# Kernel optimization log

Hardware: AMD Instinct MI355X
Metric: run time of the kernel (lower is better)

The kernel has to match this reference:

```python
import jax, jax.numpy as jnp
import numpy as np

N, M, D, O = 16384, 4096, 256, 256

def setup_inputs() -> dict:
    key = jax.random.key(0)
    k1, k2, k3, k4, k5, k6, k7 = jax.random.split(key, 7)
    H_fine = jax.random.normal(k1, (N, D), dtype=jnp.float32)
    H_coarse = jax.random.normal(k2, (M, D), dtype=jnp.float32)
    inter_channel_adj = jax.random.randint(k3, (N, M), 0, 2).astype(jnp.float32)
    # attention = nn.Linear(2D, 1): weight vector [2D], bias scalar
    wa = jax.random.normal(k4, (2 * D,), dtype=jnp.float32) * (1.0 / np.sqrt(2 * D))
    ba = jax.random.normal(k5, (1,), dtype=jnp.float32) * 0.01
    # transform = nn.Linear(D, O), xavier_uniform weight
    lim = np.sqrt(6.0 / (D + O)).astype(np.float32)
    Wt = jax.random.uniform(k6, (O, D), minval=-lim, maxval=lim, dtype=jnp.float32)
    bt = jax.random.normal(k7, (O,), dtype=jnp.float32) * 0.01
    return {"H_fine": H_fine, "H_coarse": H_coarse,
            "inter_channel_adj": inter_channel_adj,
            "wa": wa, "ba": ba, "Wt": Wt, "bt": bt}

def reference(H_fine, H_coarse, inter_channel_adj, wa, ba, Wt, bt):
    d = H_fine.shape[-1]
    # additive attention: score_ij = [hf_i ; hc_j] . wa + b
    # = hf_i . wa[:d] + hc_j . wa[d:] + b  (avoids [N,M,2D] concat)
    sf = H_fine @ wa[:d]            # [N]
    sc = H_coarse @ wa[d:]          # [M]
    scores = sf[:, None] + sc[None, :] + ba[0]        # [N, M]
    masked = scores * inter_channel_adj               # [N, M]
    weights = jax.nn.softmax(masked, axis=-1)         # [N, M]
    attn_out = weights @ H_coarse                     # [N, D]
    attn_out = attn_out + H_fine                      # add_self=True
    out = attn_out @ Wt.T + bt                        # [N, O]
    return jax.nn.relu(out)
```

## Files before the change

### kernel.cpp

```cpp
#include <hip/hip_runtime.h>
#include <hip/hip_bf16.h>
#include <stdint.h>

#define N_ 16384
#define M_ 4096
#define D_ 256
#define O_ 256

#define WS_T    0
#define WS_U    65536
#define WS_R    81920
#define WS_WTP  98304
#define WS_BP   229376

typedef float  f32x4  __attribute__((ext_vector_type(4)));
typedef short  short8 __attribute__((ext_vector_type(8)));

__device__ __forceinline__ unsigned short f2bf(float f) {
  uint32_t u = __float_as_uint(f);
  u += 0x7FFFu + ((u >> 16) & 1u);
  return (unsigned short)(u >> 16);
}
__device__ __forceinline__ uint32_t cvtpk(float a, float b) {
  __hip_bfloat162 h = __float22bfloat162_rn(float2{a, b});
  uint32_t u;
  __builtin_memcpy(&u, &h, 4);
  return u;
}

__global__ __launch_bounds__(256) void rowdot_exp_kernel(
    const float* __restrict__ X, const float* __restrict__ w,
    const float* __restrict__ bias, float* __restrict__ outv) {
  int wv = threadIdx.x >> 6, lane = threadIdx.x & 63;
  int row = blockIdx.x * 4 + wv;
  const float4* x4 = (const float4*)(X + (size_t)row * D_);
  const float4* w4 = (const float4*)w;
  float4 xa = x4[lane], wa4 = w4[lane];
  float s = xa.x * wa4.x + xa.y * wa4.y + xa.z * wa4.z + xa.w * wa4.w;
#pragma unroll
  for (int off = 32; off > 0; off >>= 1) s += __shfl_xor(s, off);
  if (lane == 0) outv[row] = expf(s + (bias ? bias[0] : 0.0f));
}

__global__ __launch_bounds__(256) void hc_pack_kernel(
    const float* __restrict__ Hc, unsigned short* __restrict__ BP,
    float* __restrict__ R) {
  __shared__ float tile[64][65];
  __shared__ float red[4][64];
  int bk = blockIdx.x >> 2;
  int bc = blockIdx.x & 3;
  int k0 = bk * 64, col0 = bc * 64;
  int t = threadIdx.x;
  int lane = t & 63, wv = t >> 6;
  int m = lane & 15, q = lane >> 4;
  float colsum = 0.0f;
#pragma unroll
  for (int i = 0; i < 16; ++i) {
    int e = t + 256 * i;
    int kk = e >> 6, cc = e & 63;
    float v = Hc[(size_t)(k0 + kk) * D_ + col0 + cc];
    tile[kk][cc] = v;
    colsum += v;
  }
  red[wv][t & 63] = colsum;
  __syncthreads();
  if (t < 64)
    atomicAdd(&R[col0 + t], red[0][t] + red[1][t] + red[2][t] + red[3][t]);
#pragma unroll
  for (int t8 = 0; t8 < 2; ++t8) {
    int tile_id = t8 * 4 + wv;
    int sub = tile_id >> 2, g = tile_id & 3;
    int kgg = bk * 2 + sub;
    int cgg = bc * 4 + g;
    short8 v8;
#pragma unroll
    for (int j = 0; j < 8; ++j)
      v8[j] = (short)f2bf(tile[sub * 32 + q * 8 + j][g * 16 + m]);
    *(short8*)(BP + ((size_t)(kgg * 16 + cgg) * 64 + lane) * 8) = v8;
  }
}

__global__ __launch_bounds__(256) void wt_pack_kernel(
    const float* __restrict__ Wt, unsigned short* __restrict__ WtP) {
  int t = blockIdx.x * 256 + threadIdx.x;
  int lane = t & 63, cg = (t >> 6) & 15, kg = t >> 10;
  int m = lane & 15, q = lane >> 4;
  const float* src = Wt + (size_t)(cg * 16 + m) * D_ + kg * 32 + q * 8;
  float4 w0 = *(const float4*)src, w1 = *(const float4*)(src + 4);
  short8 v8;
  v8[0] = (short)f2bf(w0.x); v8[1] = (short)f2bf(w0.y);
  v8[2] = (short)f2bf(w0.z); v8[3] = (short)f2bf(w0.w);
  v8[4] = (short)f2bf(w1.x); v8[5] = (short)f2bf(w1.y);
  v8[6] = (short)f2bf(w1.z); v8[7] = (short)f2bf(w1.w);
  *(short8*)(WtP + (size_t)t * 8) = v8;
}

__device__ __forceinline__ short8 transform8(float4 A0, float4 A1, float t,
                                             float4 u0, float4 u1, float& rs) {
  float p0 = fmaf(A0.x, t * u0.x, -A0.x);
  float p1 = fmaf(A0.y, t * u0.y, -A0.y);
  float p2 = fmaf(A0.z, t * u0.z, -A0.z);
  float p3 = fmaf(A0.w, t * u0.w, -A0.w);
  float p4 = fmaf(A1.x, t * u1.x, -A1.x);
  float p5 = fmaf(A1.y, t * u1.y, -A1.y);
  float p6 = fmaf(A1.z, t * u1.z, -A1.z);
  float p7 = fmaf(A1.w, t * u1.w, -A1.w);
  rs += ((p0 + p1) + (p2 + p3)) + ((p4 + p5) + (p6 + p7));
  union { short8 s; uint32_t u[4]; } r;
  r.u[0] = cvtpk(p0, p1);
  r.u[1] = cvtpk(p2, p3);
  r.u[2] = cvtpk(p4, p5);
  r.u[3] = cvtpk(p6, p7);
  return r.s;
}

__global__ __launch_bounds__(512, 4) void fused_kernel(
    const float* __restrict__ adj, const unsigned short* __restrict__ BP,
    const float* __restrict__ tv, const float* __restrict__ uv,
    const float* __restrict__ Rv, const float* __restrict__ Hf,
    const unsigned short* __restrict__ WtP, const float* __restrict__ bt,
    float* __restrict__ out) {
  __shared__ float u_lds[M_];
  __shared__ float part[32][260];
  __shared__ float redd[2][32];
  __shared__ float Lrow[32];
  __shared__ alignas(16) unsigned short attn[32][264];

  int tid = threadIdx.x;
  int w = tid >> 6, lane = tid & 63;
  int q = lane >> 4, m = lane & 15;
  int colq = w & 3, khalf = w >> 2;
  int i0 = blockIdx.x * 32;

  for (int i = tid; i < M_; i += 512) u_lds[i] = uv[i];
  {
    float* pz = &part[0][0];
    for (int i = tid; i < 32 * 260; i += 512) pz[i] = 0.0f;
  }

  float t0 = tv[i0 + m], t1 = tv[i0 + 16 + m];
  const float* a0 = adj + (size_t)(i0 + m) * M_ + khalf * 2048 + q * 8;
  const float* a1 = a0 + (size_t)16 * M_;
  const unsigned short* bb =
      BP + ((size_t)(khalf * 64) * 16 + colq * 4) * 512 + (size_t)lane * 8;
  const float* ub = u_lds + khalf * 2048 + q * 8;

  f32x4 acc[2][4];
#pragma unroll
  for (int s = 0; s < 2; ++s)
#pragma unroll
    for (int n = 0; n < 4; ++n) acc[s][n] = (f32x4){0.f, 0.f, 0.f, 0.f};
  float rs0 = 0.0f, rs1 = 0.0f;

  __syncthreads();

  float4 xa0 = *(const float4*)(a0);
  float4 xa1 = *(const float4*)(a0 + 4);
  float4 xb0 = *(const float4*)(a1);
  float4 xb1 = *(const float4*)(a1 + 4);
  float4 ya0 = *(const float4*)(a0 + 32);
  float4 ya1 = *(const float4*)(a0 + 36);
  float4 yb0 = *(const float4*)(a1 + 32);
  float4 yb1 = *(const float4*)(a1 + 36);
  short8 BX[4], BY[4];
#pragma unroll
  for (int n = 0; n < 4; ++n) BX[n] = *(const short8*)(bb + n * 512);
#pragma unroll
  for (int n = 0; n < 4; ++n) BY[n] = *(const short8*)(bb + 8192 + n * 512);

  for (int kk = 0; kk < 64; kk += 2) {
    {
      int k2 = (kk + 2) & 63;
      float4 na0 = *(const float4*)(a0 + k2 * 32);
      float4 na1 = *(const float4*)(a0 + k2 * 32 + 4);
      float4 nb0 = *(const float4*)(a1 + k2 * 32);
      float4 nb1 = *(const float4*)(a1 + k2 * 32 + 4);
      short8 nB[4];
#pragma unroll
      for (int n = 0; n < 4; ++n)
        nB[n] = *(const short8*)(bb + (size_t)k2 * 8192 + n * 512);

      float4 u0 = *(const float4*)(ub + kk * 32);
      float4 u1 = *(const float4*)(ub + kk * 32 + 4);
      short8 af0 = transform8(xa0, xa1, t0, u0, u1, rs0);
      short8 af1 = transform8(xb0, xb1, t1, u0, u1, rs1);
#pragma unroll
      for (int n = 0; n < 4; ++n) {
        acc[0][n] = __builtin_amdgcn_mfma_f32_16x16x32_bf16(af0, BX[n], acc[0][n], 0, 0, 0);
        acc[1][n] = __builtin_amdgcn_mfma_f32_16x16x32_bf16(af1, BX[n], acc[1][n], 0, 0, 0);
      }
      xa0 = na0; xa1 = na1; xb0 = nb0; xb1 = nb1;
#pragma unroll
      for (int n = 0; n < 4; ++n) BX[n] = nB[n];
    }
    {
      int k3 = (kk + 3) & 63;
      float4 na0 = *(const float4*)(a0 + k3 * 32);
      float4 na1 = *(const float4*)(a0 + k3 * 32 + 4);
      float4 nb0 = *(const float4*)(a1 + k3 * 32);
      float4 nb1 = *(const float4*)(a1 + k3 * 32 + 4);
      short8 nB[4];
#pragma unroll
      for (int n = 0; n < 4; ++n)
        nB[n] = *(const short8*)(bb + (size_t)k3 * 8192 + n * 512);

      float4 u0 = *(const float4*)(ub + (kk + 1) * 32);
      float4 u1 = *(const float4*)(ub + (kk + 1) * 32 + 4);
      short8 af0 = transform8(ya0, ya1, t0, u0, u1, rs0);
      short8 af1 = transform8(yb0, yb1, t1, u0, u1, rs1);
#pragma unroll
      for (int n = 0; n < 4; ++n) {
        acc[0][n] = __builtin_amdgcn_mfma_f32_16x16x32_bf16(af0, BY[n], acc[0][n], 0, 0, 0);
        acc[1][n] = __builtin_amdgcn_mfma_f32_16x16x32_bf16(af1, BY[n], acc[1][n], 0, 0, 0);
      }
      ya0 = na0; ya1 = na1; yb0 = nb0; yb1 = nb1;
#pragma unroll
      for (int n = 0; n < 4; ++n) BY[n] = nB[n];
    }
  }

  rs0 += __shfl_xor(rs0, 16); rs0 += __shfl_xor(rs0, 32);
  rs1 += __shfl_xor(rs1, 16); rs1 += __shfl_xor(rs1, 32);
  if (colq == 0 && lane < 16) {
    redd[khalf][m] = rs0;
    redd[khalf][16 + m] = rs1;
  }

#pragma unroll
  for (int s = 0; s < 2; ++s)
#pragma unroll
    for (int n = 0; n < 4; ++n) {
      int col = colq * 64 + n * 16 + m;
#pragma unroll
      for (int r = 0; r < 4; ++r)
        atomicAdd(&part[s * 16 + q * 4 + r][col], acc[s][n][r]);
    }
  __syncthreads();

  if (tid < 32) Lrow[tid] = redd[0][tid] + redd[1][tid];
  __syncthreads();

#pragma unroll
  for (int rr = 0; rr < 4; ++rr) {
    int r = w * 4 + rr;
    float invL = 1.0f / (Lrow[r] + (float)M_);
    size_t grow = (size_t)(i0 + r) * D_;
#pragma unroll
    for (int h = 0; h < 2; ++h) {
      int c = h * 128 + 2 * lane;
      float2 pv = *(const float2*)&part[r][c];
      float2 rv = *(const float2*)(Rv + c);
      float2 hv = *(const float2*)(Hf + grow + c);
      float v0 = fmaf(pv.x + rv.x, invL, hv.x);
      float v1 = fmaf(pv.y + rv.y, invL, hv.y);
      *(uint32_t*)&attn[r][c] = cvtpk(v0, v1);
    }
  }
  __syncthreads();

  int rtile = w & 1, c64 = w >> 1;
  f32x4 facc[4];
#pragma unroll
  for (int n = 0; n < 4; ++n) facc[n] = (f32x4){0.f, 0.f, 0.f, 0.f};
#pragma unroll
  for (int kf = 0; kf < 8; ++kf) {
    short8 af = *(const short8*)&attn[rtile * 16 + m][kf * 32 + q * 8];
#pragma unroll
    for (int n = 0; n < 4; ++n) {
      int cg = c64 * 4 + n;
      short8 bf = *(const short8*)(WtP + ((size_t)(kf * 16 + cg) * 64 + lane) * 8);
      facc[n] = __builtin_amdgcn_mfma_f32_16x16x32_bf16(af, bf, facc[n], 0, 0, 0);
    }
  }
#pragma unroll
  for (int n = 0; n < 4; ++n) {
    int col = c64 * 64 + n * 16 + m;
    float b = bt[col];
#pragma unroll
    for (int r = 0; r < 4; ++r) {
      size_t row = (size_t)i0 + rtile * 16 + q * 4 + r;
      out[row * O_ + col] = fmaxf(facc[n][r] + b, 0.0f);
    }
  }
}

extern "C" void kernel_launch(void* const* d_in, const int* in_sizes, int n_in,
                              void* d_out, int out_size, void* d_ws, size_t ws_size,
                              hipStream_t stream) {
  const float* Hf  = (const float*)d_in[0];
  const float* Hc  = (const float*)d_in[1];
  const float* adj = (const float*)d_in[2];
  const float* wa  = (const float*)d_in[3];
  const float* ba  = (const float*)d_in[4];
  const float* Wt  = (const float*)d_in[5];
  const float* bt  = (const float*)d_in[6];
  float* out = (float*)d_out;

  char* ws = (char*)d_ws;
  float* tv = (float*)(ws + WS_T);
  float* uv = (float*)(ws + WS_U);
  float* Rv = (float*)(ws + WS_R);
  unsigned short* WtP = (unsigned short*)(ws + WS_WTP);
  unsigned short* BP  = (unsigned short*)(ws + WS_BP);

  hipMemsetAsync(Rv, 0, D_ * sizeof(float), stream);

  rowdot_exp_kernel<<<N_ / 4, 256, 0, stream>>>(Hf, wa, ba, tv);
  rowdot_exp_kernel<<<M_ / 4, 256, 0, stream>>>(Hc, wa + D_, nullptr, uv);
  hc_pack_kernel<<<256, 256, 0, stream>>>(Hc, BP, Rv);
  wt_pack_kernel<<<32, 256, 0, stream>>>(Wt, WtP);

  fused_kernel<<<N_ / 32, 512, 0, stream>>>(adj, BP, tv, uv, Rv, Hf, WtP, bt, out);
}
```

Measured before the change: 522.1 us.

## Pre-pack adjacency into bitmask and compute row sums in separate pass

Adds a pass that reads the fp32 adjacency once, writes a packed bitmask via ballot and computes the per-row softmax denominator. The GEMM kernel then rebuilds bf16 A fragments from the bits and the t·u-1 coefficients, so the adjacency is no longer streamed inside the MFMA loop. This separates the bandwidth-bound scan from the compute loop and shrinks LDS use by unioning buffers. The cost is an extra kernel launch and the 8 MB bitmask written and read back. The full 268 MB adjacency read remains, just moved to a simpler streaming kernel.

After: 510.6 us. 1.02x faster.

```diff
diff --git a/kernel.cpp b/kernel.cpp
--- a/kernel.cpp
+++ b/kernel.cpp
@@ -10,8 +10,10 @@
 #define WS_T    0
 #define WS_U    65536
 #define WS_R    81920
-#define WS_WTP  98304
-#define WS_BP   229376
+#define WS_LSUM 98304
+#define WS_WTP  163840
+#define WS_BP   294912
+#define WS_ABM  2457600
 
 typedef float  f32x4  __attribute__((ext_vector_type(4)));
 typedef short  short8 __attribute__((ext_vector_type(8)));
@@ -95,36 +97,88 @@
   *(short8*)(WtP + (size_t)t * 8) = v8;
 }
 
-__device__ __forceinline__ short8 transform8(float4 A0, float4 A1, float t,
-                                             float4 u0, float4 u1, float& rs) {
-  float p0 = fmaf(A0.x, t * u0.x, -A0.x);
-  float p1 = fmaf(A0.y, t * u0.y, -A0.y);
-  float p2 = fmaf(A0.z, t * u0.z, -A0.z);
-  float p3 = fmaf(A0.w, t * u0.w, -A0.w);
-  float p4 = fmaf(A1.x, t * u1.x, -A1.x);
-  float p5 = fmaf(A1.y, t * u1.y, -A1.y);
-  float p6 = fmaf(A1.z, t * u1.z, -A1.z);
-  float p7 = fmaf(A1.w, t * u1.w, -A1.w);
-  rs += ((p0 + p1) + (p2 + p3)) + ((p4 + p5) + (p6 + p7));
+__global__ __launch_bounds__(256) void pack_bits_kernel(
+    const float* __restrict__ adj, const float* __restrict__ tv,
+    const float* __restrict__ uv, unsigned long long* __restrict__ ABM,
+    float* __restrict__ Lsum) {
+  __shared__ float u_lds[M_];
+  int tid = threadIdx.x;
+  int w = tid >> 6, lane = tid & 63;
+  for (int i = tid; i < M_; i += 256) u_lds[i] = uv[i];
+  __syncthreads();
+  int gw = blockIdx.x * 4 + w;
+
+#pragma unroll 1
+  for (int rr = 0; rr < 4; ++rr) {
+    int r = gw * 4 + rr;
+    const float* ar = adj + (size_t)r * M_;
+    float su = 0.0f, sc = 0.0f;
+    float x0 = ar[lane], x1 = ar[64 + lane], x2 = ar[128 + lane], x3 = ar[192 + lane];
+#pragma unroll 1
+    for (int i = 0; i < 16; ++i) {
+      int k0 = i * 256;
+      int k1 = (i + 1 < 16) ? k0 + 256 : 0;
+      float n0 = ar[k1 + lane];
+      float n1 = ar[k1 + 64 + lane];
+      float n2 = ar[k1 + 128 + lane];
+      float n3 = ar[k1 + 192 + lane];
+      unsigned long long b0 = __ballot(x0 != 0.0f);
+      unsigned long long b1 = __ballot(x1 != 0.0f);
+      unsigned long long b2 = __ballot(x2 != 0.0f);
+      unsigned long long b3 = __ballot(x3 != 0.0f);
+      su = fmaf(x0, u_lds[k0 + lane], su);
+      su = fmaf(x1, u_lds[k0 + 64 + lane], su);
+      su = fmaf(x2, u_lds[k0 + 128 + lane], su);
+      su = fmaf(x3, u_lds[k0 + 192 + lane], su);
+      sc += (x0 + x1) + (x2 + x3);
+      if (lane < 4) {
+        unsigned long long bb = lane == 0 ? b0 : lane == 1 ? b1 : lane == 2 ? b2 : b3;
+        ABM[(size_t)r * 64 + i * 4 + lane] = bb;
+      }
+      x0 = n0; x1 = n1; x2 = n2; x3 = n3;
+    }
+#pragma unroll
+    for (int off = 32; off > 0; off >>= 1) {
+      su += __shfl_xor(su, off);
+      sc += __shfl_xor(sc, off);
+    }
+    if (lane == 0) Lsum[r] = tv[r] * su - sc;
+  }
+}
+
+__device__ __forceinline__ short8 frag_bits(uint32_t bits, float t,
+                                            float4 u0, float4 u1) {
+  float c[8];
+  c[0] = fmaf(t, u0.x, -1.0f); c[1] = fmaf(t, u0.y, -1.0f);
+  c[2] = fmaf(t, u0.z, -1.0f); c[3] = fmaf(t, u0.w, -1.0f);
+  c[4] = fmaf(t, u1.x, -1.0f); c[5] = fmaf(t, u1.y, -1.0f);
+  c[6] = fmaf(t, u1.z, -1.0f); c[7] = fmaf(t, u1.w, -1.0f);
   union { short8 s; uint32_t u[4]; } r;
-  r.u[0] = cvtpk(p0, p1);
-  r.u[1] = cvtpk(p2, p3);
-  r.u[2] = cvtpk(p4, p5);
-  r.u[3] = cvtpk(p6, p7);
+#pragma unroll
+  for (int p = 0; p < 4; ++p) {
+    uint32_t mlo = 0u - ((bits >> (2 * p)) & 1u);
+    uint32_t mhi = 0u - ((bits >> (2 * p + 1)) & 1u);
+    r.u[p] = cvtpk(c[2 * p], c[2 * p + 1]) &
+             ((mlo & 0x0000FFFFu) | (mhi & 0xFFFF0000u));
+  }
   return r.s;
 }
 
-__global__ __launch_bounds__(512, 4) void fused_kernel(
-    const float* __restrict__ adj, const unsigned short* __restrict__ BP,
+__global__ __launch_bounds__(512, 4) void gemm_kernel(
+    const unsigned int* __restrict__ ABM32, const unsigned short* __restrict__ BP,
     const float* __restrict__ tv, const float* __restrict__ uv,
-    const float* __restrict__ Rv, const float* __restrict__ Hf,
-    const unsigned short* __restrict__ WtP, const float* __restrict__ bt,
-    float* __restrict__ out) {
-  __shared__ float u_lds[M_];
+    const float* __restrict__ Lsum, const float* __restrict__ Rv,
+    const float* __restrict__ Hf, const unsigned short* __restrict__ WtP,
+    const float* __restrict__ bt, float* __restrict__ out) {
+  union SM {
+    struct {
+      float u[M_];
+      unsigned int bt[128][32];
+    } s;
+    unsigned short attn[32][264];
+  };
+  __shared__ SM sm;
   __shared__ float part[32][260];
-  __shared__ float redd[2][32];
-  __shared__ float Lrow[32];
-  __shared__ alignas(16) unsigned short attn[32][264];
 
   int tid = threadIdx.x;
   int w = tid >> 6, lane = tid & 63;
@@ -132,36 +186,29 @@
   int colq = w & 3, khalf = w >> 2;
   int i0 = blockIdx.x * 32;
 
-  for (int i = tid; i < M_; i += 512) u_lds[i] = uv[i];
+  for (int i = tid; i < M_; i += 512) sm.s.u[i] = uv[i];
+  for (int p = tid; p < 32 * 128; p += 512) {
+    int row = p >> 7, word = p & 127;
+    sm.s.bt[word][row] = ABM32[(size_t)(i0 + row) * 128 + word];
+  }
   {
     float* pz = &part[0][0];
     for (int i = tid; i < 32 * 260; i += 512) pz[i] = 0.0f;
   }
 
   float t0 = tv[i0 + m], t1 = tv[i0 + 16 + m];
-  const float* a0 = adj + (size_t)(i0 + m) * M_ + khalf * 2048 + q * 8;
-  const float* a1 = a0 + (size_t)16 * M_;
   const unsigned short* bb =
       BP + ((size_t)(khalf * 64) * 16 + colq * 4) * 512 + (size_t)lane * 8;
-  const float* ub = u_lds + khalf * 2048 + q * 8;
+  int kgbase = khalf * 64;
 
   f32x4 acc[2][4];
 #pragma unroll
   for (int s = 0; s < 2; ++s)
 #pragma unroll
     for (int n = 0; n < 4; ++n) acc[s][n] = (f32x4){0.f, 0.f, 0.f, 0.f};
-  float rs0 = 0.0f, rs1 = 0.0f;
-
-  __syncthreads();
-
-  float4 xa0 = *(const float4*)(a0);
-  float4 xa1 = *(const float4*)(a0 + 4);
-  float4 xb0 = *(const float4*)(a1);
-  float4 xb1 = *(const float4*)(a1 + 4);
-  float4 ya0 = *(const float4*)(a0 + 32);
-  float4 ya1 = *(const float4*)(a0 + 36);
-  float4 yb0 = *(const float4*)(a1 + 32);
-  float4 yb1 = *(const float4*)(a1 + 36);
+
+  __syncthreads();
+
   short8 BX[4], BY[4];
 #pragma unroll
   for (int n = 0; n < 4; ++n) BX[n] = *(const short8*)(bb + n * 512);
@@ -171,59 +218,46 @@
   for (int kk = 0; kk < 64; kk += 2) {
     {
       int k2 = (kk + 2) & 63;
-      float4 na0 = *(const float4*)(a0 + k2 * 32);
-      float4 na1 = *(const float4*)(a0 + k2 * 32 + 4);
-      float4 nb0 = *(const float4*)(a1 + k2 * 32);
-      float4 nb1 = *(const float4*)(a1 + k2 * 32 + 4);
       short8 nB[4];
 #pragma unroll
       for (int n = 0; n < 4; ++n)
         nB[n] = *(const short8*)(bb + (size_t)k2 * 8192 + n * 512);
-
-      float4 u0 = *(const float4*)(ub + kk * 32);
-      float4 u1 = *(const float4*)(ub + kk * 32 + 4);
-      short8 af0 = transform8(xa0, xa1, t0, u0, u1, rs0);
-      short8 af1 = transform8(xb0, xb1, t1, u0, u1, rs1);
+      int kg = kgbase + kk;
+      uint32_t w0 = sm.s.bt[kg][m];
+      uint32_t w1 = sm.s.bt[kg][16 + m];
+      float4 u0 = *(const float4*)&sm.s.u[kg * 32 + q * 8];
+      float4 u1 = *(const float4*)&sm.s.u[kg * 32 + q * 8 + 4];
+      short8 af0 = frag_bits((w0 >> (q * 8)) & 0xffu, t0, u0, u1);
+      short8 af1 = frag_bits((w1 >> (q * 8)) & 0xffu, t1, u0, u1);
 #pragma unroll
       for (int n = 0; n < 4; ++n) {
         acc[0][n] = __builtin_amdgcn_mfma_f32_16x16x32_bf16(af0, BX[n], acc[0][n], 0, 0, 0);
         acc[1][n] = __builtin_amdgcn_mfma_f32_16x16x32_bf16(af1, BX[n], acc[1][n], 0, 0, 0);
       }
-      xa0 = na0; xa1 = na1; xb0 = nb0; xb1 = nb1;
 #pragma unroll
       for (int n = 0; n < 4; ++n) BX[n] = nB[n];
     }
     {
       int k3 = (kk + 3) & 63;
-      float4 na0 = *(const float4*)(a0 + k3 * 32);
-      float4 na1 = *(const float4*)(a0 + k3 * 32 + 4);
-      float4 nb0 = *(const float4*)(a1 + k3 * 32);
-      float4 nb1 = *(const float4*)(a1 + k3 * 32 + 4);
       short8 nB[4];
 #pragma unroll
       for (int n = 0; n < 4; ++n)
         nB[n] = *(const short8*)(bb + (size_t)k3 * 8192 + n * 512);
-
-      float4 u0 = *(const float4*)(ub + (kk + 1) * 32);
-      float4 u1 = *(const float4*)(ub + (kk + 1) * 32 + 4);
-      short8 af0 = transform8(ya0, ya1, t0, u0, u1, rs0);
-      short8 af1 = transform8(yb0, yb1, t1, u0, u1, rs1);
+      int kg = kgbase + kk + 1;
+      uint32_t w0 = sm.s.bt[kg][m];
+      uint32_t w1 = sm.s.bt[kg][16 + m];
+      float4 u0 = *(const float4*)&sm.s.u[kg * 32 + q * 8];
+      float4 u1 = *(const float4*)&sm.s.u[kg * 32 + q * 8 + 4];
+      short8 af0 = frag_bits((w0 >> (q * 8)) & 0xffu, t0, u0, u1);
+      short8 af1 = frag_bits((w1 >> (q * 8)) & 0xffu, t1, u0, u1);
 #pragma unroll
       for (int n = 0; n < 4; ++n) {
         acc[0][n] = __builtin_amdgcn_mfma_f32_16x16x32_bf16(af0, BY[n], acc[0][n], 0, 0, 0);
         acc[1][n] = __builtin_amdgcn_mfma_f32_16x16x32_bf16(af1, BY[n], acc[1][n], 0, 0, 0);
       }
-      ya0 = na0; ya1 = na1; yb0 = nb0; yb1 = nb1;
 #pragma unroll
       for (int n = 0; n < 4; ++n) BY[n] = nB[n];
     }
-  }
-
-  rs0 += __shfl_xor(rs0, 16); rs0 += __shfl_xor(rs0, 32);
-  rs1 += __shfl_xor(rs1, 16); rs1 += __shfl_xor(rs1, 32);
-  if (colq == 0 && lane < 16) {
-    redd[khalf][m] = rs0;
-    redd[khalf][16 + m] = rs1;
   }
 
 #pragma unroll
@@ -237,23 +271,20 @@
     }
   __syncthreads();
 
-  if (tid < 32) Lrow[tid] = redd[0][tid] + redd[1][tid];
-  __syncthreads();
-
 #pragma unroll
   for (int rr = 0; rr < 4; ++rr) {
     int r = w * 4 + rr;
-    float invL = 1.0f / (Lrow[r] + (float)M_);
+    float invL = 1.0f / (Lsum[i0 + r] + (float)M_);
     size_t grow = (size_t)(i0 + r) * D_;
 #pragma unroll
     for (int h = 0; h < 2; ++h) {
       int c = h * 128 + 2 * lane;
       float2 pv = *(const float2*)&part[r][c];
-      float2 rv = *(const float2*)(Rv + c);
+      float2 rv2 = *(const float2*)(Rv + c);
       float2 hv = *(const float2*)(Hf + grow + c);
-      float v0 = fmaf(pv.x + rv.x, invL, hv.x);
-      float v1 = fmaf(pv.y + rv.y, invL, hv.y);
-      *(uint32_t*)&attn[r][c] = cvtpk(v0, v1);
+      float v0 = fmaf(pv.x + rv2.x, invL, hv.x);
+      float v1 = fmaf(pv.y + rv2.y, invL, hv.y);
+      *(uint32_t*)&sm.attn[r][c] = cvtpk(v0, v1);
     }
   }
   __syncthreads();
@@ -264,7 +295,7 @@
   for (int n = 0; n < 4; ++n) facc[n] = (f32x4){0.f, 0.f, 0.f, 0.f};
 #pragma unroll
   for (int kf = 0; kf < 8; ++kf) {
-    short8 af = *(const short8*)&attn[rtile * 16 + m][kf * 32 + q * 8];
+    short8 af = *(const short8*)&sm.attn[rtile * 16 + m][kf * 32 + q * 8];
 #pragma unroll
     for (int n = 0; n < 4; ++n) {
       int cg = c64 * 4 + n;
@@ -297,11 +328,13 @@
   float* out = (float*)d_out;
 
   char* ws = (char*)d_ws;
-  float* tv = (float*)(ws + WS_T);
-  float* uv = (float*)(ws + WS_U);
-  float* Rv = (float*)(ws + WS_R);
+  float* tv   = (float*)(ws + WS_T);
+  float* uv   = (float*)(ws + WS_U);
+  float* Rv   = (float*)(ws + WS_R);
+  float* Lsum = (float*)(ws + WS_LSUM);
   unsigned short* WtP = (unsigned short*)(ws + WS_WTP);
   unsigned short* BP  = (unsigned short*)(ws + WS_BP);
+  unsigned long long* ABM = (unsigned long long*)(ws + WS_ABM);
 
   hipMemsetAsync(Rv, 0, D_ * sizeof(float), stream);
 
@@ -310,5 +343,7 @@
   hc_pack_kernel<<<256, 256, 0, stream>>>(Hc, BP, Rv);
   wt_pack_kernel<<<32, 256, 0, stream>>>(Wt, WtP);
 
-  fused_kernel<<<N_ / 32, 512, 0, stream>>>(adj, BP, tv, uv, Rv, Hf, WtP, bt, out);
-}
+  pack_bits_kernel<<<1024, 256, 0, stream>>>(adj, tv, uv, ABM, Lsum);
+  gemm_kernel<<<N_ / 32, 512, 0, stream>>>((const unsigned int*)ABM, BP, tv, uv,
+                                           Lsum, Rv, Hf, WtP, bt, out);
+}
```
